# Optimization experiments

Hardware: AMD Instinct MI355X
Metric: run time of the kernel (lower is better)

Reference implementation:

```python
import jax, jax.numpy as jnp
import numpy as np

N = 50000      # nodes
E = 800000     # edges
INIT = 256     # input feature dim
HID = 64       # per-head hidden dim
EMB = 128      # output embed dim
H = 8          # heads
ALPHA = 0.2    # leaky-relu slope
EPS = 1e-16    # guard for isolated nodes


def setup_inputs() -> dict:
    key = jax.random.key(0)
    ks = jax.random.split(key, 6)
    x = jax.random.normal(ks[0], (N, INIT), dtype=jnp.float32)
    edge_index = jax.random.randint(ks[1], (2, E), 0, N, dtype=jnp.int32)
    # xavier-ish scaling keeps exp(-leakyrelu(.)) in a sane range
    W1 = jax.random.normal(ks[2], (H, INIT, HID), dtype=jnp.float32) / np.sqrt(INIT).astype(np.float32)
    a1 = jax.random.normal(ks[3], (H, 2 * HID), dtype=jnp.float32) / np.sqrt(2 * HID).astype(np.float32)
    Wo = jax.random.normal(ks[4], (H * HID, EMB), dtype=jnp.float32) / np.sqrt(H * HID).astype(np.float32)
    ao = jax.random.normal(ks[5], (2 * EMB,), dtype=jnp.float32) / np.sqrt(2 * EMB).astype(np.float32)
    return {"x": x, "edge_index": edge_index, "W1": W1, "a1": a1, "Wo": Wo, "ao": ao}


def _sp_att_head(x, W, a, src, dst):
    """One sparse GAT head (pyGAT SpGraphAttentionLayer math)."""
    h = x @ W                                              # [N, F']
    eh = jnp.concatenate([h[src], h[dst]], axis=1)          # [E, 2F']
    ee = jnp.exp(-jax.nn.leaky_relu(eh @ a, ALPHA))         # [E]
    denom = jax.ops.segment_sum(ee, src, num_segments=N) + EPS          # [N]
    num = jax.ops.segment_sum(ee[:, None] * h[dst], src, num_segments=N)  # [N, F']
    h_prime = num / denom[:, None]
    att = ee / denom[src]
    return h_prime, att


def reference(x, edge_index, W1, a1, Wo, ao, args=0):
    src, dst = edge_index[0], edge_index[1]
    # first (and only) multi-head layer, concat=True -> elu per head, concat on feature dim
    heads = [jax.nn.elu(_sp_att_head(x, W1[i], a1[i], src, dst)[0]) for i in range(H)]
    x1 = jnp.concatenate(heads, axis=1)                     # [N, H*HID]
    # output attention layer, concat=False; top-level applies elu
    h_prime, att_out = _sp_att_head(x1, Wo, ao, src, dst)
    return jax.nn.elu(h_prime), edge_index, att_out
```

## Files before the change

### kernel.cpp

```cpp
#include <hip/hip_runtime.h>
#include <hip/hip_bf16.h>
#include <cstddef>

#define NN    50000
#define NE    800000
#define FIN   256
#define HID   64
#define NH    8
#define F1    512
#define EMB   128
#define ALPHA 0.2f
#define EPSF  1e-16f
#define NBLK  ((NN + 255) / 256)

#if defined(__has_builtin)
# if __has_builtin(__builtin_amdgcn_cvt_scalef32_pk_f32_fp4) && __has_builtin(__builtin_amdgcn_cvt_scalef32_pk_fp4_f32)
#  define HAVE_FP4 1
# else
#  define HAVE_FP4 0
# endif
#else
# define HAVE_FP4 0
#endif

typedef __hip_bfloat16 bf16;
typedef __attribute__((ext_vector_type(8))) short short8;
typedef __attribute__((ext_vector_type(4))) float f32x4;
typedef __attribute__((ext_vector_type(2))) float f32x2;

#if HAVE_FP4
typedef uint2 pay_t;
#define PAYB1 (F1 / 2)
#define PAYB2 (EMB / 2)
#define SINV1 2.0f
#define SINV2 4.0f
#define PSC1  0.5f
#define PSC2  0.25f
#else
typedef uint4 pay_t;
#define PAYB1 F1
#define PAYB2 EMB
#define SINV1 1.0f
#define SINV2 1.0f
#define PSC1  1.0f
#define PSC2  1.0f
#endif

__device__ __forceinline__ float eluf(float x){ return x > 0.f ? x : __expf(x) - 1.f; }
__device__ __forceinline__ float lrelu_neg_exp(float s){
    float lr = s > 0.f ? s : ALPHA * s;
    return __expf(-lr);
}
__device__ __forceinline__ float b2f(unsigned u){ return __uint_as_float(u << 16); }

__device__ __forceinline__ void fma16pk(f32x2* acc, pay_t q, float e){
    f32x2 e2; e2[0] = e; e2[1] = e;
#if HAVE_FP4
    acc[0] += __builtin_amdgcn_cvt_scalef32_pk_f32_fp4(q.x, 1.0f, 0) * e2;
    acc[1] += __builtin_amdgcn_cvt_scalef32_pk_f32_fp4(q.x, 1.0f, 1) * e2;
    acc[2] += __builtin_amdgcn_cvt_scalef32_pk_f32_fp4(q.x, 1.0f, 2) * e2;
    acc[3] += __builtin_amdgcn_cvt_scalef32_pk_f32_fp4(q.x, 1.0f, 3) * e2;
    acc[4] += __builtin_amdgcn_cvt_scalef32_pk_f32_fp4(q.y, 1.0f, 0) * e2;
    acc[5] += __builtin_amdgcn_cvt_scalef32_pk_f32_fp4(q.y, 1.0f, 1) * e2;
    acc[6] += __builtin_amdgcn_cvt_scalef32_pk_f32_fp4(q.y, 1.0f, 2) * e2;
    acc[7] += __builtin_amdgcn_cvt_scalef32_pk_f32_fp4(q.y, 1.0f, 3) * e2;
#else
    acc[0] += __builtin_amdgcn_cvt_pk_f32_fp8(q.x, false) * e2;
    acc[1] += __builtin_amdgcn_cvt_pk_f32_fp8(q.x, true)  * e2;
    acc[2] += __builtin_amdgcn_cvt_pk_f32_fp8(q.y, false) * e2;
    acc[3] += __builtin_amdgcn_cvt_pk_f32_fp8(q.y, true)  * e2;
    acc[4] += __builtin_amdgcn_cvt_pk_f32_fp8(q.z, false) * e2;
    acc[5] += __builtin_amdgcn_cvt_pk_f32_fp8(q.z, true)  * e2;
    acc[6] += __builtin_amdgcn_cvt_pk_f32_fp8(q.w, false) * e2;
    acc[7] += __builtin_amdgcn_cvt_pk_f32_fp8(q.w, true)  * e2;
#endif
}

__device__ __forceinline__ unsigned bpack(float a, float b){
    unsigned ua = __float_as_uint(a), ub = __float_as_uint(b);
    ua = (ua + 0x7fffu + ((ua >> 16) & 1)) >> 16;
    ub = (ub + 0x7fffu + ((ub >> 16) & 1)) >> 16;
    return (ua & 0xffffu) | (ub << 16);
}

__global__ void k_tw1(const float* __restrict__ W1, bf16* __restrict__ Bt1){
    int i = blockIdx.x * 256 + threadIdx.x;
    if (i >= F1 * FIN) return;
    int n = i >> 8, k = i & 255;
    Bt1[i] = __float2bfloat16(W1[(size_t)(n >> 6) * FIN * HID + (size_t)k * HID + (n & 63)]);
}

__global__ void k_tw2(const float* __restrict__ Wo, bf16* __restrict__ WoT){
    int i = blockIdx.x * 256 + threadIdx.x;
    if (i >= EMB * F1) return;
    int n = i >> 9, k = i & 511;
    WoT[i] = __float2bfloat16(Wo[(size_t)k * EMB + n]);
}

__global__ void k_q4(const unsigned char* __restrict__ in, unsigned* __restrict__ out,
                     int n8, float sinv){
    int i = blockIdx.x * 256 + threadIdx.x;
    if (i >= n8) return;
    uint2 v = *(const uint2*)(in + (size_t)i * 8);
#if HAVE_FP4
    f32x2 a = __builtin_amdgcn_cvt_pk_f32_fp8(v.x, false);
    f32x2 b = __builtin_amdgcn_cvt_pk_f32_fp8(v.x, true);
    f32x2 c = __builtin_amdgcn_cvt_pk_f32_fp8(v.y, false);
    f32x2 d = __builtin_amdgcn_cvt_pk_f32_fp8(v.y, true);
    unsigned r = 0;
    r = __builtin_amdgcn_cvt_scalef32_pk_fp4_f32(r, a[0] * sinv, a[1] * sinv, 1.0f, 0);
    r = __builtin_amdgcn_cvt_scalef32_pk_fp4_f32(r, b[0] * sinv, b[1] * sinv, 1.0f, 1);
    r = __builtin_amdgcn_cvt_scalef32_pk_fp4_f32(r, c[0] * sinv, c[1] * sinv, 1.0f, 2);
    r = __builtin_amdgcn_cvt_scalef32_pk_fp4_f32(r, d[0] * sinv, d[1] * sinv, 1.0f, 3);
    out[i] = r;
#else
    (void)sinv;
    *(uint2*)((unsigned char*)out + (size_t)i * 8) = v;
#endif
}

__global__ void k_zero(int* p, int n){
    int i = blockIdx.x * 256 + threadIdx.x;
    if (i < n) p[i] = 0;
}

__global__ void k_count(const int* __restrict__ src, int* __restrict__ cnt){
    int e = blockIdx.x * 256 + threadIdx.x;
    if (e < NE) atomicAdd(&cnt[src[e]], 1);
}

__global__ __launch_bounds__(256) void k_bsum(const int* __restrict__ cnt, int* __restrict__ bsum){
    const int b = blockIdx.x, t = threadIdx.x, idx = b * 256 + t;
    int v = (idx < NN) ? cnt[idx] : 0;
#pragma unroll
    for (int o = 1; o < 64; o <<= 1) v += __shfl_xor(v, o);
    __shared__ int ws[4];
    if ((t & 63) == 0) ws[t >> 6] = v;
    __syncthreads();
    if (t == 0) bsum[b] = ws[0] + ws[1] + ws[2] + ws[3];
}

__global__ __launch_bounds__(256) void k_scanb(const int* __restrict__ bsum,
                                               int* __restrict__ boff,
                                               int* __restrict__ rp){
    const int t = threadIdx.x;
    __shared__ int s[256];
    const int v = (t < NBLK) ? bsum[t] : 0;
    s[t] = v;
    __syncthreads();
    for (int o = 1; o < 256; o <<= 1){
        int u = (t >= o) ? s[t - o] : 0;
        __syncthreads();
        s[t] += u;
        __syncthreads();
    }
    if (t < NBLK) boff[t] = s[t] - v;
    if (t == 255) rp[NN] = s[255];
}

__global__ __launch_bounds__(256) void k_rp(const int* __restrict__ cnt,
                                            const int* __restrict__ boff,
                                            int* __restrict__ rp){
    const int b = blockIdx.x, t = threadIdx.x, idx = b * 256 + t;
    const int v = (idx < NN) ? cnt[idx] : 0;
    __shared__ int s[256];
    s[t] = v;
    __syncthreads();
    for (int o = 1; o < 256; o <<= 1){
        int u = (t >= o) ? s[t - o] : 0;
        __syncthreads();
        s[t] += u;
        __syncthreads();
    }
    if (idx < NN) rp[idx] = boff[b] + s[t] - v;
}

__global__ void k_scatter_ee(const int* __restrict__ src, const int* __restrict__ dst,
                             const int* __restrict__ rp, int* __restrict__ cur,
                             const float* __restrict__ s11, const float* __restrict__ s12,
                             int* __restrict__ sdst, int* __restrict__ ssrc,
                             unsigned short* __restrict__ ee8b){
    int e = blockIdx.x * 256 + threadIdx.x;
    if (e >= NE) return;
    int s = src[e], d = dst[e];
    int p = atomicAdd(&cur[s], 1);
    int pos = rp[s] + p;
    sdst[pos] = d;
    ssrc[pos] = s;
    const float* ps = s11 + (size_t)s * NH;
    const float* pd = s12 + (size_t)d * NH;
    float w[8];
#pragma unroll
    for (int h = 0; h < 8; h++) w[h] = lrelu_neg_exp(ps[h] + pd[h]);
    uint4 o;
    o.x = bpack(w[0], w[1]); o.y = bpack(w[2], w[3]);
    o.z = bpack(w[4], w[5]); o.w = bpack(w[6], w[7]);
    *(uint4*)(ee8b + (size_t)pos * 8) = o;
}

__global__ void k_ee2(const int* __restrict__ ssrc, const int* __restrict__ sdst,
                      const float* __restrict__ s21, const float* __restrict__ s22,
                      float* __restrict__ ee2){
    int i = blockIdx.x * 256 + threadIdx.x;
    if (i >= NE) return;
    ee2[i] = lrelu_neg_exp(s21[ssrc[i]] + s22[sdst[i]]);
}

__global__ __launch_bounds__(256) void k_gemm1f(const float* __restrict__ A,
                                                const bf16* __restrict__ B,
                                                unsigned char* __restrict__ C){
    constexpr int K = FIN, N = F1;
    constexpr int LDT = 40;
    __shared__ __align__(16) bf16 As[128 * LDT];
    __shared__ __align__(16) bf16 Bs[128 * LDT];
    const int t = threadIdx.x;
    const int lane = t & 63, wid = t >> 6;
    const int m0 = blockIdx.x * 128, n0 = blockIdx.y * 128;
    const int r0 = t >> 2, u0 = t & 3;
    const int r1 = r0 + 64;
    const int rb = (wid & 1) * 64, cb = (wid >> 1) * 64;
    const int fr = lane & 15, fk = (lane >> 4) * 8;

    f32x4 acc[4][4];
#pragma unroll
    for (int i = 0; i < 4; i++)
#pragma unroll
        for (int j = 0; j < 4; j++) acc[i][j] = (f32x4)(0.f);

    for (int k0 = 0; k0 < K; k0 += 32){
        const int ga0 = m0 + r0, ga1 = m0 + r1;
        float4 a0a = make_float4(0,0,0,0), a0b = a0a, a1a = a0a, a1b = a0a;
        if (ga0 < NN){
            const float* p = A + (size_t)ga0 * K + k0 + u0 * 8;
            a0a = *(const float4*)p; a0b = *(const float4*)(p + 4);
        }
        if (ga1 < NN){
            const float* p = A + (size_t)ga1 * K + k0 + u0 * 8;
            a1a = *(const float4*)p; a1b = *(const float4*)(p + 4);
        }
        uint4 av0, av1;
        av0.x = bpack(a0a.x, a0a.y); av0.y = bpack(a0a.z, a0a.w);
        av0.z = bpack(a0b.x, a0b.y); av0.w = bpack(a0b.z, a0b.w);
        av1.x = bpack(a1a.x, a1a.y); av1.y = bpack(a1a.z, a1a.w);
        av1.z = bpack(a1b.x, a1b.y); av1.w = bpack(a1b.z, a1b.w);
        uint4 bv0 = *(const uint4*)(B + (size_t)(n0 + r0) * K + k0 + u0 * 8);
        uint4 bv1 = *(const uint4*)(B + (size_t)(n0 + r1) * K + k0 + u0 * 8);
        __syncthreads();
        *(uint4*)(As + r0 * LDT + u0 * 8) = av0;
        *(uint4*)(As + r1 * LDT + u0 * 8) = av1;
        *(uint4*)(Bs + r0 * LDT + u0 * 8) = bv0;
        *(uint4*)(Bs + r1 * LDT + u0 * 8) = bv1;
        __syncthreads();
        short8 af[4], bf_[4];
#pragma unroll
        for (int i = 0; i < 4; i++){
            af[i]  = *(const short8*)(As + (rb + i * 16 + fr) * LDT + fk);
            bf_[i] = *(const short8*)(Bs + (cb + i * 16 + fr) * LDT + fk);
        }
#pragma unroll
        for (int i = 0; i < 4; i++)
#pragma unroll
            for (int j = 0; j < 4; j++)
                acc[i][j] = __builtin_amdgcn_mfma_f32_16x16x32_bf16(af[i], bf_[j], acc[i][j], 0, 0, 0);
    }
    const int crow = m0 + rb + (lane >> 4) * 4;
    const int ccol = n0 + cb + (lane & 15);
#pragma unroll
    for (int i = 0; i < 4; i++)
#pragma unroll
        for (int j = 0; j < 4; j++)
#pragma unroll
            for (int v = 0; v < 4; v++){
                int row = crow + i * 16 + v;
                if (row < NN){
                    float val = acc[i][j][v];
                    unsigned r = __builtin_amdgcn_cvt_pk_fp8_f32(val, val, 0u, false);
                    C[(size_t)row * N + ccol + j * 16] = (unsigned char)(r & 0xffu);
                }
            }
}

__global__ __launch_bounds__(256) void k_gemm2n(const bf16* __restrict__ A,
                                                const bf16* __restrict__ B,
                                                unsigned char* __restrict__ C){
    constexpr int K = F1, N = EMB;
    constexpr int LDT = 40;
    __shared__ __align__(16) bf16 As[64 * LDT];
    __shared__ __align__(16) bf16 Bs[128 * LDT];
    const int t = threadIdx.x;
    const int lane = t & 63, wid = t >> 6;
    const int m0 = blockIdx.x * 64;
    const int r = t >> 2, u0 = t & 3;
    const int rb = (wid & 1) * 32, cb = (wid >> 1) * 64;
    const int fr = lane & 15, fk = (lane >> 4) * 8;

    f32x4 acc[2][4];
#pragma unroll
    for (int i = 0; i < 2; i++)
#pragma unroll
        for (int j = 0; j < 4; j++) acc[i][j] = (f32x4)(0.f);

    for (int k0 = 0; k0 < K; k0 += 32){
        const int ga = m0 + r;
        uint4 av = (ga < NN) ? *(const uint4*)(A + (size_t)ga * K + k0 + u0 * 8)
                             : make_uint4(0, 0, 0, 0);
        uint4 bv0 = *(const uint4*)(B + (size_t)r * K + k0 + u0 * 8);
        uint4 bv1 = *(const uint4*)(B + (size_t)(r + 64) * K + k0 + u0 * 8);
        __syncthreads();
        *(uint4*)(As + r * LDT + u0 * 8) = av;
        *(uint4*)(Bs + r * LDT + u0 * 8) = bv0;
        *(uint4*)(Bs + (r + 64) * LDT + u0 * 8) = bv1;
        __syncthreads();
        short8 af[2], bf_[4];
#pragma unroll
        for (int i = 0; i < 2; i++)
            af[i] = *(const short8*)(As + (rb + i * 16 + fr) * LDT + fk);
#pragma unroll
        for (int j = 0; j < 4; j++)
            bf_[j] = *(const short8*)(Bs + (cb + j * 16 + fr) * LDT + fk);
#pragma unroll
        for (int i = 0; i < 2; i++)
#pragma unroll
            for (int j = 0; j < 4; j++)
                acc[i][j] = __builtin_amdgcn_mfma_f32_16x16x32_bf16(af[i], bf_[j], acc[i][j], 0, 0, 0);
    }
    const int crow = m0 + rb + (lane >> 4) * 4;
    const int ccol = cb + (lane & 15);
#pragma unroll
    for (int i = 0; i < 2; i++)
#pragma unroll
        for (int j = 0; j < 4; j++)
#pragma unroll
            for (int v = 0; v < 4; v++){
                int row = crow + i * 16 + v;
                if (row < NN){
                    float val = acc[i][j][v];
                    unsigned r8 = __builtin_amdgcn_cvt_pk_fp8_f32(val, val, 0u, false);
                    C[(size_t)row * N + ccol + j * 16] = (unsigned char)(r8 & 0xffu);
                }
            }
}

__global__ void k_s1q(const unsigned char* __restrict__ h1q, const float* __restrict__ a1,
                      float* __restrict__ s11, float* __restrict__ s12,
                      unsigned char* __restrict__ pay){
    int idx = blockIdx.x * 256 + threadIdx.x;
    if (idx >= NN * NH) return;
    int n = idx >> 3, h = idx & 7;
    const uint4* hp = (const uint4*)(h1q + (size_t)n * F1 + h * HID);
    const float* a  = a1 + (size_t)h * 2 * HID;
    float d1 = 0.f, d2 = 0.f;
#if HAVE_FP4
    unsigned w8[8];
#endif
#pragma unroll
    for (int u = 0; u < 4; u++){
        uint4 q = hp[u];
        int j = u * 16;
        f32x2 p0 = __builtin_amdgcn_cvt_pk_f32_fp8(q.x, false);
        f32x2 p1 = __builtin_amdgcn_cvt_pk_f32_fp8(q.x, true);
        f32x2 p2 = __builtin_amdgcn_cvt_pk_f32_fp8(q.y, false);
        f32x2 p3 = __builtin_amdgcn_cvt_pk_f32_fp8(q.y, true);
        f32x2 p4 = __builtin_amdgcn_cvt_pk_f32_fp8(q.z, false);
        f32x2 p5 = __builtin_amdgcn_cvt_pk_f32_fp8(q.z, true);
        f32x2 p6 = __builtin_amdgcn_cvt_pk_f32_fp8(q.w, false);
        f32x2 p7 = __builtin_amdgcn_cvt_pk_f32_fp8(q.w, true);
        d1 += p0[0]*a[j+0] + p0[1]*a[j+1] + p1[0]*a[j+2] + p1[1]*a[j+3]
            + p2[0]*a[j+4] + p2[1]*a[j+5] + p3[0]*a[j+6] + p3[1]*a[j+7]
            + p4[0]*a[j+8] + p4[1]*a[j+9] + p5[0]*a[j+10]+ p5[1]*a[j+11]
            + p6[0]*a[j+12]+ p6[1]*a[j+13]+ p7[0]*a[j+14]+ p7[1]*a[j+15];
        d2 += p0[0]*a[HID+j+0] + p0[1]*a[HID+j+1] + p1[0]*a[HID+j+2] + p1[1]*a[HID+j+3]
            + p2[0]*a[HID+j+4] + p2[1]*a[HID+j+5] + p3[0]*a[HID+j+6] + p3[1]*a[HID+j+7]
            + p4[0]*a[HID+j+8] + p4[1]*a[HID+j+9] + p5[0]*a[HID+j+10]+ p5[1]*a[HID+j+11]
            + p6[0]*a[HID+j+12]+ p6[1]*a[HID+j+13]+ p7[0]*a[HID+j+14]+ p7[1]*a[HID+j+15];
#if HAVE_FP4
        unsigned r0 = 0, r1 = 0;
        r0 = __builtin_amdgcn_cvt_scalef32_pk_fp4_f32(r0, p0[0]*SINV1, p0[1]*SINV1, 1.0f, 0);
        r0 = __builtin_amdgcn_cvt_scalef32_pk_fp4_f32(r0, p1[0]*SINV1, p1[1]*SINV1, 1.0f, 1);
        r0 = __builtin_amdgcn_cvt_scalef32_pk_fp4_f32(r0, p2[0]*SINV1, p2[1]*SINV1, 1.0f, 2);
        r0 = __builtin_amdgcn_cvt_scalef32_pk_fp4_f32(r0, p3[0]*SINV1, p3[1]*SINV1, 1.0f, 3);
        r1 = __builtin_amdgcn_cvt_scalef32_pk_fp4_f32(r1, p4[0]*SINV1, p4[1]*SINV1, 1.0f, 0);
        r1 = __builtin_amdgcn_cvt_scalef32_pk_fp4_f32(r1, p5[0]*SINV1, p5[1]*SINV1, 1.0f, 1);
        r1 = __builtin_amdgcn_cvt_scalef32_pk_fp4_f32(r1, p6[0]*SINV1, p6[1]*SINV1, 1.0f, 2);
        r1 = __builtin_amdgcn_cvt_scalef32_pk_fp4_f32(r1, p7[0]*SINV1, p7[1]*SINV1, 1.0f, 3);
        w8[2 * u] = r0; w8[2 * u + 1] = r1;
#endif
    }
    s11[idx] = d1;
    s12[idx] = d2;
#if HAVE_FP4
    uint4* op = (uint4*)(pay + (size_t)n * PAYB1 + h * (HID / 2));
    uint4 o0, o1;
    o0.x = w8[0]; o0.y = w8[1]; o0.z = w8[2]; o0.w = w8[3];
    o1.x = w8[4]; o1.y = w8[5]; o1.z = w8[6]; o1.w = w8[7];
    op[0] = o0; op[1] = o1;
#else
    uint4* op = (uint4*)(pay + (size_t)n * PAYB1 + h * HID);
    op[0] = hp[0]; op[1] = hp[1]; op[2] = hp[2]; op[3] = hp[3];
#endif
}

__global__ __launch_bounds__(256) void k_agg1(const unsigned char* __restrict__ hq,
                                              const unsigned short* __restrict__ ee8b,
                                              const int* __restrict__ rp,
                                              const int* __restrict__ sdst,
                                              bf16* __restrict__ x1){
    const int t = threadIdx.x, lane = t & 63, w = t >> 6;
    const int n = blockIdx.x * 4 + w;
    const int l32 = lane & 31;
    const int half = lane >> 5;
    const int hf = l32 >> 2;
    const int eslot = lane >> 3;
    f32x2 acc[8];
#pragma unroll
    for (int i = 0; i < 8; i++){ acc[i][0] = 0.f; acc[i][1] = 0.f; }
    float dedp = 0.f;
    const int start = rp[n], end = rp[n + 1];
    const unsigned char* __restrict__ hl = hq + (size_t)l32 * (PAYB1 / 32);
    for (int c0 = start; c0 < end; c0 += 64){
        const int m = min(64, end - c0);
        int dreg = (lane < m) ? sdst[c0 + lane] : 0;
        for (int g = 0; g * 8 < m; g++){
            unsigned short eu = ee8b[(size_t)(c0 + g * 8) * 8 + lane];
            dedp += (g * 8 + eslot < m) ? b2f(eu) : 0.f;
        }
        for (int j = 0; j < m; j += 16){
            int dj[8]; unsigned short eu[8]; pay_t q[8];
#pragma unroll
            for (int p = 0; p < 8; p++){
                const int e2 = j + 2 * p + half;
                dj[p] = __shfl(dreg, e2);
                eu[p] = ee8b[(size_t)(c0 + e2) * 8 + hf];
                q[p]  = *(const pay_t*)(hl + (size_t)dj[p] * PAYB1);
            }
#pragma unroll
            for (int p = 0; p < 8; p++){
                const int e2 = j + 2 * p + half;
                const float e = (e2 < m) ? b2f(eu[p]) : 0.f;
                fma16pk(acc, q[p], e);
            }
        }
    }
    dedp += __shfl_xor(dedp, 8);
    dedp += __shfl_xor(dedp, 16);
    dedp += __shfl_xor(dedp, 32);
#pragma unroll
    for (int i = 0; i < 8; i++){
        acc[i][0] += __shfl_xor(acc[i][0], 32);
        acc[i][1] += __shfl_xor(acc[i][1], 32);
    }
    float ded = __shfl(dedp, hf);
    const float inv = PSC1 / (ded + EPSF);
    if (half == 0){
        float o[16];
#pragma unroll
        for (int i = 0; i < 8; i++){
            o[2 * i]     = eluf(acc[i][0] * inv);
            o[2 * i + 1] = eluf(acc[i][1] * inv);
        }
        uint4 ov0, ov1;
        ov0.x = bpack(o[0], o[1]);   ov0.y = bpack(o[2], o[3]);
        ov0.z = bpack(o[4], o[5]);   ov0.w = bpack(o[6], o[7]);
        ov1.x = bpack(o[8], o[9]);   ov1.y = bpack(o[10], o[11]);
        ov1.z = bpack(o[12], o[13]); ov1.w = bpack(o[14], o[15]);
        bf16* xp = x1 + (size_t)n * F1 + l32 * 16;
        *(uint4*)xp = ov0;
        *(uint4*)(xp + 8) = ov1;
    }
}

__global__ void k_s2(const unsigned char* __restrict__ h2q, const float* __restrict__ ao,
                     float* __restrict__ s21, float* __restrict__ s22){
    int n = blockIdx.x * 256 + threadIdx.x;
    if (n >= NN) return;
    const uint4* hp = (const uint4*)(h2q + (size_t)n * EMB);
    float d1 = 0.f, d2 = 0.f;
#pragma unroll
    for (int u = 0; u < 8; u++){
        uint4 q = hp[u];
        int j = u * 16;
#define S2(w, o) { f32x2 p0 = __builtin_amdgcn_cvt_pk_f32_fp8((w), false); \
                   f32x2 p1 = __builtin_amdgcn_cvt_pk_f32_fp8((w), true); \
                   d1 += p0[0]*ao[(o)] + p0[1]*ao[(o)+1] + p1[0]*ao[(o)+2] + p1[1]*ao[(o)+3]; \
                   d2 += p0[0]*ao[EMB+(o)] + p0[1]*ao[EMB+(o)+1] + p1[0]*ao[EMB+(o)+2] + p1[1]*ao[EMB+(o)+3]; }
        S2(q.x, j) S2(q.y, j + 4) S2(q.z, j + 8) S2(q.w, j + 12)
#undef S2
    }
    s21[n] = d1;
    s22[n] = d2;
}

__global__ __launch_bounds__(256) void k_agg2(const unsigned char* __restrict__ hq,
                                              const float* __restrict__ ee2,
                                              const int* __restrict__ rp,
                                              const int* __restrict__ sdst,
                                              float* __restrict__ den2,
                                              float* __restrict__ out0){
    const int t = threadIdx.x, lane = t & 63, w = t >> 6;
    const int n = blockIdx.x * 4 + w;
    const int slot = lane >> 3;
    const int fpos = lane & 7;
    f32x2 acc[8];
#pragma unroll
    for (int i = 0; i < 8; i++){ acc[i][0] = 0.f; acc[i][1] = 0.f; }
    float dedp = 0.f;
    const int start = rp[n], end = rp[n + 1];
    const unsigned char* __restrict__ hl = hq + (size_t)fpos * (PAYB2 / 8);
    for (int c0 = start; c0 < end; c0 += 64){
        const int m = min(64, end - c0);
        int dreg = (lane < m) ? sdst[c0 + lane] : 0;
        float ev = (lane < m) ? ee2[c0 + lane] : 0.f;
        dedp += ev;
        for (int j = 0; j < m; j += 8){
            const int ei = j + slot;
            const float e = __shfl(ev, ei);
            const int   d = __shfl(dreg, ei);
            pay_t q = *(const pay_t*)(hl + (size_t)d * PAYB2);
            fma16pk(acc, q, e);
        }
    }
#pragma unroll
    for (int o = 1; o <= 32; o <<= 1) dedp += __shfl_xor(dedp, o);
#pragma unroll
    for (int o = 8; o <= 32; o <<= 1)
#pragma unroll
        for (int i = 0; i < 8; i++){
            acc[i][0] += __shfl_xor(acc[i][0], o);
            acc[i][1] += __shfl_xor(acc[i][1], o);
        }
    const float den = dedp + EPSF;
    if (slot == 0){
        const float inv = PSC2 / den;
        float* op = out0 + (size_t)n * EMB + fpos * 16;
#pragma unroll
        for (int u = 0; u < 4; u++){
            float4 ov;
            ov.x = eluf(acc[2 * u][0] * inv);
            ov.y = eluf(acc[2 * u][1] * inv);
            ov.z = eluf(acc[2 * u + 1][0] * inv);
            ov.w = eluf(acc[2 * u + 1][1] * inv);
            *(float4*)(op + u * 4) = ov;
        }
        if (lane == 0) den2[n] = den;
    }
}

__global__ void k_att_edge4(const int* __restrict__ ei,
                            const float* __restrict__ s21, const float* __restrict__ s22,
                            const float* __restrict__ den2,
                            float* __restrict__ outE, float* __restrict__ outA){
    int i = blockIdx.x * 256 + threadIdx.x;
    if (i >= NE / 4) return;
    int4 s4 = ((const int4*)ei)[i];
    int4 d4 = ((const int4*)(ei + NE))[i];
    float4 fs = make_float4((float)s4.x, (float)s4.y, (float)s4.z, (float)s4.w);
    float4 fd = make_float4((float)d4.x, (float)d4.y, (float)d4.z, (float)d4.w);
    ((float4*)outE)[i] = fs;
    ((float4*)(outE + NE))[i] = fd;
    float4 av;
    av.x = lrelu_neg_exp(s21[s4.x] + s22[d4.x]) / den2[s4.x];
    av.y = lrelu_neg_exp(s21[s4.y] + s22[d4.y]) / den2[s4.y];
    av.z = lrelu_neg_exp(s21[s4.z] + s22[d4.z]) / den2[s4.z];
    av.w = lrelu_neg_exp(s21[s4.w] + s22[d4.w]) / den2[s4.w];
    ((float4*)outA)[i] = av;
}

extern "C" void kernel_launch(void* const* d_in, const int* in_sizes, int n_in,
                              void* d_out, int out_size, void* d_ws, size_t ws_size,
                              hipStream_t stream){
    const float* x  = (const float*)d_in[0];
    const int*   ei = (const int*)d_in[1];
    const float* W1 = (const float*)d_in[2];
    const float* a1 = (const float*)d_in[3];
    const float* Wo = (const float*)d_in[4];
    const float* ao = (const float*)d_in[5];
    float* out = (float*)d_out;
    const int* src = ei;
    const int* dst = ei + NE;

    char* w = (char*)d_ws;
    auto alloc = [&](size_t bytes) -> char* {
        char* p = w;
        w += (bytes + 255) & ~(size_t)255;
        return p;
    };
    unsigned char* h1pay = (unsigned char*)alloc((size_t)NN * F1);
    bf16*  x1   = (bf16*) alloc((size_t)NN * F1 * 2);
    unsigned char* h1q = (unsigned char*)alloc((size_t)NN * F1);
    unsigned char* h2q = (unsigned char*)alloc((size_t)NN * EMB);
    unsigned short* ee8b = (unsigned short*)alloc(((size_t)NE + 64) * 8 * 2);
    float* ee2  = (float*)alloc((size_t)NE * 4);
    bf16*  Bt1  = (bf16*) alloc((size_t)F1 * FIN * 2);
    bf16*  WoT  = (bf16*) alloc((size_t)EMB * F1 * 2);
    float* s11  = (float*)alloc((size_t)NN * NH * 4);
    float* s12  = (float*)alloc((size_t)NN * NH * 4);
    float* s21  = (float*)alloc((size_t)NN * 4);
    float* s22  = (float*)alloc((size_t)NN * 4);
    float* den2 = (float*)alloc((size_t)NN * 4);
    int*   cnt2 = (int*)  alloc((size_t)2 * NN * 4);
    int*   rp   = (int*)  alloc((size_t)(NN + 1) * 4);
    int*   sdst = (int*)  alloc((size_t)NE * 4);
    int*   ssrc = (int*)  alloc((size_t)NE * 4);
    int*   bsum = (int*)  alloc((size_t)NBLK * 4);
    int*   boff = (int*)  alloc((size_t)NBLK * 4);
    int*   cnt = cnt2;
    int*   cur = cnt2 + NN;
    unsigned char* h2pay = (unsigned char*)x1;

    k_tw1<<<(F1 * FIN + 255) / 256, 256, 0, stream>>>(W1, Bt1);
    k_tw2<<<(EMB * F1 + 255) / 256, 256, 0, stream>>>(Wo, WoT);

    k_zero <<<(2 * NN + 255) / 256, 256, 0, stream>>>(cnt2, 2 * NN);
    k_count<<<(NE + 255) / 256,     256, 0, stream>>>(src, cnt);
    k_bsum <<<NBLK,                 256, 0, stream>>>(cnt, bsum);
    k_scanb<<<1,                    256, 0, stream>>>(bsum, boff, rp);
    k_rp   <<<NBLK,                 256, 0, stream>>>(cnt, boff, rp);

    k_gemm1f<<<dim3((NN + 127) / 128, F1 / 128), 256, 0, stream>>>(x, Bt1, h1q);
    k_s1q <<<(NN * NH + 255) / 256, 256, 0, stream>>>(h1q, a1, s11, s12, h1pay);
    k_scatter_ee<<<(NE + 255) / 256, 256, 0, stream>>>(src, dst, rp, cur, s11, s12,
                                                       sdst, ssrc, ee8b);
    k_agg1<<<NN / 4, 256, 0, stream>>>(h1pay, ee8b, rp, sdst, x1);

    k_gemm2n<<<(NN + 63) / 64, 256, 0, stream>>>(x1, WoT, h2q);
    k_q4  <<<(NN * EMB / 8 + 255) / 256, 256, 0, stream>>>(h2q, (unsigned*)h2pay, NN * EMB / 8, SINV2);
    k_s2  <<<(NN + 255) / 256, 256, 0, stream>>>(h2q, ao, s21, s22);
    k_ee2 <<<(NE + 255) / 256, 256, 0, stream>>>(ssrc, sdst, s21, s22, ee2);
    k_agg2<<<NN / 4, 256, 0, stream>>>(h2pay, ee2, rp, sdst, den2, out);

    k_att_edge4<<<(NE / 4 + 255) / 256, 256, 0, stream>>>(ei, s21, s22, den2,
                                                          out + (size_t)NN * EMB,
                                                          out + (size_t)NN * EMB + 2 * NE);
}
```

Measured before the change: 319.7 us.

## Pack per-edge CSR data into interleaved 32-byte records

Replaces the separate sorted dst, src, bf16 attention and layer-2 score arrays with one 32-byte record per sorted edge holding dst, src, the layer-2 score and eight packed layer-1 weights. The scatter, ee2 and both aggregation kernels read and write these records, so each edge's data comes from one or two adjacent 16-byte loads instead of several arrays. Layer-1 denominators are now summed per head across the whole wave and then selected, rather than reduced with a strided layout. In exchange the per-edge footprint grows to 32 bytes, with padding, so total traffic may rise. The per-head bf16 reads in k_agg1 now stride 32 bytes instead of 16.

```diff
diff --git a/kernel.cpp b/kernel.cpp
--- a/kernel.cpp
+++ b/kernel.cpp
@@ -45,6 +45,8 @@
 #define PSC1  1.0f
 #define PSC2  1.0f
 #endif
+
+#define RECB 32
 
 __device__ __forceinline__ float eluf(float x){ return x > 0.f ? x : __expf(x) - 1.f; }
 __device__ __forceinline__ float lrelu_neg_exp(float s){
@@ -178,32 +180,35 @@
 __global__ void k_scatter_ee(const int* __restrict__ src, const int* __restrict__ dst,
                              const int* __restrict__ rp, int* __restrict__ cur,
                              const float* __restrict__ s11, const float* __restrict__ s12,
-                             int* __restrict__ sdst, int* __restrict__ ssrc,
-                             unsigned short* __restrict__ ee8b){
+                             unsigned char* __restrict__ rec){
     int e = blockIdx.x * 256 + threadIdx.x;
     if (e >= NE) return;
     int s = src[e], d = dst[e];
-    int p = atomicAdd(&cur[s], 1);
-    int pos = rp[s] + p;
-    sdst[pos] = d;
-    ssrc[pos] = s;
     const float* ps = s11 + (size_t)s * NH;
     const float* pd = s12 + (size_t)d * NH;
     float w[8];
 #pragma unroll
     for (int h = 0; h < 8; h++) w[h] = lrelu_neg_exp(ps[h] + pd[h]);
-    uint4 o;
-    o.x = bpack(w[0], w[1]); o.y = bpack(w[2], w[3]);
-    o.z = bpack(w[4], w[5]); o.w = bpack(w[6], w[7]);
-    *(uint4*)(ee8b + (size_t)pos * 8) = o;
-}
-
-__global__ void k_ee2(const int* __restrict__ ssrc, const int* __restrict__ sdst,
-                      const float* __restrict__ s21, const float* __restrict__ s22,
-                      float* __restrict__ ee2){
+    uint4 rB;
+    rB.x = bpack(w[0], w[1]); rB.y = bpack(w[2], w[3]);
+    rB.z = bpack(w[4], w[5]); rB.w = bpack(w[6], w[7]);
+    uint4 rA;
+    rA.x = (unsigned)d; rA.y = (unsigned)s; rA.z = 0u; rA.w = 0u;
+    int p = atomicAdd(&cur[s], 1);
+    size_t pos = (size_t)rp[s] + p;
+    uint4* rq = (uint4*)(rec + pos * RECB);
+    rq[0] = rA;
+    rq[1] = rB;
+}
+
+__global__ void k_ee2(unsigned char* __restrict__ rec,
+                      const float* __restrict__ s21, const float* __restrict__ s22){
     int i = blockIdx.x * 256 + threadIdx.x;
     if (i >= NE) return;
-    ee2[i] = lrelu_neg_exp(s21[ssrc[i]] + s22[sdst[i]]);
+    const uint4 rA = *(const uint4*)(rec + (size_t)i * RECB);
+    int d = (int)rA.x, s = (int)rA.y;
+    float v = lrelu_neg_exp(s21[s] + s22[d]);
+    *(float*)(rec + (size_t)i * RECB + 8) = v;
 }
 
 __global__ __launch_bounds__(256) void k_gemm1f(const float* __restrict__ A,
@@ -401,36 +406,42 @@
 }
 
 __global__ __launch_bounds__(256) void k_agg1(const unsigned char* __restrict__ hq,
-                                              const unsigned short* __restrict__ ee8b,
+                                              const unsigned char* __restrict__ rec,
                                               const int* __restrict__ rp,
-                                              const int* __restrict__ sdst,
                                               bf16* __restrict__ x1){
     const int t = threadIdx.x, lane = t & 63, w = t >> 6;
     const int n = blockIdx.x * 4 + w;
     const int l32 = lane & 31;
     const int half = lane >> 5;
     const int hf = l32 >> 2;
-    const int eslot = lane >> 3;
     f32x2 acc[8];
 #pragma unroll
     for (int i = 0; i < 8; i++){ acc[i][0] = 0.f; acc[i][1] = 0.f; }
-    float dedp = 0.f;
+    float ded8[8];
+#pragma unroll
+    for (int h = 0; h < 8; h++) ded8[h] = 0.f;
     const int start = rp[n], end = rp[n + 1];
     const unsigned char* __restrict__ hl = hq + (size_t)l32 * (PAYB1 / 32);
     for (int c0 = start; c0 < end; c0 += 64){
         const int m = min(64, end - c0);
-        int dreg = (lane < m) ? sdst[c0 + lane] : 0;
-        for (int g = 0; g * 8 < m; g++){
-            unsigned short eu = ee8b[(size_t)(c0 + g * 8) * 8 + lane];
-            dedp += (g * 8 + eslot < m) ? b2f(eu) : 0.f;
-        }
+        uint4 rA = make_uint4(0, 0, 0, 0), rB = make_uint4(0, 0, 0, 0);
+        if (lane < m){
+            const uint4* rq = (const uint4*)(rec + (size_t)(c0 + lane) * RECB);
+            rA = rq[0];
+            rB = rq[1];
+        }
+        const int dreg = (int)rA.x;
+        ded8[0] += b2f(rB.x & 0xffffu); ded8[1] += b2f(rB.x >> 16);
+        ded8[2] += b2f(rB.y & 0xffffu); ded8[3] += b2f(rB.y >> 16);
+        ded8[4] += b2f(rB.z & 0xffffu); ded8[5] += b2f(rB.z >> 16);
+        ded8[6] += b2f(rB.w & 0xffffu); ded8[7] += b2f(rB.w >> 16);
         for (int j = 0; j < m; j += 16){
             int dj[8]; unsigned short eu[8]; pay_t q[8];
 #pragma unroll
             for (int p = 0; p < 8; p++){
                 const int e2 = j + 2 * p + half;
                 dj[p] = __shfl(dreg, e2);
-                eu[p] = ee8b[(size_t)(c0 + e2) * 8 + hf];
+                eu[p] = *(const unsigned short*)(rec + (size_t)(c0 + e2) * RECB + 16 + hf * 2);
                 q[p]  = *(const pay_t*)(hl + (size_t)dj[p] * PAYB1);
             }
 #pragma unroll
@@ -441,15 +452,19 @@
             }
         }
     }
-    dedp += __shfl_xor(dedp, 8);
-    dedp += __shfl_xor(dedp, 16);
-    dedp += __shfl_xor(dedp, 32);
+#pragma unroll
+    for (int h = 0; h < 8; h++){
+#pragma unroll
+        for (int o = 1; o <= 32; o <<= 1) ded8[h] += __shfl_xor(ded8[h], o);
+    }
 #pragma unroll
     for (int i = 0; i < 8; i++){
         acc[i][0] += __shfl_xor(acc[i][0], 32);
         acc[i][1] += __shfl_xor(acc[i][1], 32);
     }
-    float ded = __shfl(dedp, hf);
+    float ded = ded8[0];
+#pragma unroll
+    for (int h = 1; h < 8; h++) ded = (hf == h) ? ded8[h] : ded;
     const float inv = PSC1 / (ded + EPSF);
     if (half == 0){
         float o[16];
@@ -491,9 +506,8 @@
 }
 
 __global__ __launch_bounds__(256) void k_agg2(const unsigned char* __restrict__ hq,
-                                              const float* __restrict__ ee2,
+                                              const unsigned char* __restrict__ rec,
                                               const int* __restrict__ rp,
-                                              const int* __restrict__ sdst,
                                               float* __restrict__ den2,
                                               float* __restrict__ out0){
     const int t = threadIdx.x, lane = t & 63, w = t >> 6;
@@ -508,8 +522,10 @@
     const unsigned char* __restrict__ hl = hq + (size_t)fpos * (PAYB2 / 8);
     for (int c0 = start; c0 < end; c0 += 64){
         const int m = min(64, end - c0);
-        int dreg = (lane < m) ? sdst[c0 + lane] : 0;
-        float ev = (lane < m) ? ee2[c0 + lane] : 0.f;
+        uint4 rA = make_uint4(0, 0, 0, 0);
+        if (lane < m) rA = *(const uint4*)(rec + (size_t)(c0 + lane) * RECB);
+        const int dreg = (int)rA.x;
+        const float ev = __uint_as_float(rA.z);
         dedp += ev;
         for (int j = 0; j < m; j += 8){
             const int ei = j + slot;
@@ -584,12 +600,11 @@
         w += (bytes + 255) & ~(size_t)255;
         return p;
     };
-    unsigned char* h1pay = (unsigned char*)alloc((size_t)NN * F1);
+    unsigned char* h1pay = (unsigned char*)alloc((size_t)NN * PAYB1);
     bf16*  x1   = (bf16*) alloc((size_t)NN * F1 * 2);
     unsigned char* h1q = (unsigned char*)alloc((size_t)NN * F1);
     unsigned char* h2q = (unsigned char*)alloc((size_t)NN * EMB);
-    unsigned short* ee8b = (unsigned short*)alloc(((size_t)NE + 64) * 8 * 2);
-    float* ee2  = (float*)alloc((size_t)NE * 4);
+    unsigned char* rec = (unsigned char*)alloc(((size_t)NE + 64) * RECB);
     bf16*  Bt1  = (bf16*) alloc((size_t)F1 * FIN * 2);
     bf16*  WoT  = (bf16*) alloc((size_t)EMB * F1 * 2);
     float* s11  = (float*)alloc((size_t)NN * NH * 4);
@@ -599,8 +614,6 @@
     float* den2 = (float*)alloc((size_t)NN * 4);
     int*   cnt2 = (int*)  alloc((size_t)2 * NN * 4);
     int*   rp   = (int*)  alloc((size_t)(NN + 1) * 4);
-    int*   sdst = (int*)  alloc((size_t)NE * 4);
-    int*   ssrc = (int*)  alloc((size_t)NE * 4);
     int*   bsum = (int*)  alloc((size_t)NBLK * 4);
     int*   boff = (int*)  alloc((size_t)NBLK * 4);
     int*   cnt = cnt2;
@@ -618,15 +631,14 @@
 
     k_gemm1f<<<dim3((NN + 127) / 128, F1 / 128), 256, 0, stream>>>(x, Bt1, h1q);
     k_s1q <<<(NN * NH + 255) / 256, 256, 0, stream>>>(h1q, a1, s11, s12, h1pay);
-    k_scatter_ee<<<(NE + 255) / 256, 256, 0, stream>>>(src, dst, rp, cur, s11, s12,
-                                                       sdst, ssrc, ee8b);
-    k_agg1<<<NN / 4, 256, 0, stream>>>(h1pay, ee8b, rp, sdst, x1);
+    k_scatter_ee<<<(NE + 255) / 256, 256, 0, stream>>>(src, dst, rp, cur, s11, s12, rec);
+    k_agg1<<<NN / 4, 256, 0, stream>>>(h1pay, rec, rp, x1);
 
     k_gemm2n<<<(NN + 63) / 64, 256, 0, stream>>>(x1, WoT, h2q);
     k_q4  <<<(NN * EMB / 8 + 255) / 256, 256, 0, stream>>>(h2q, (unsigned*)h2pay, NN * EMB / 8, SINV2);
     k_s2  <<<(NN + 255) / 256, 256, 0, stream>>>(h2q, ao, s21, s22);
-    k_ee2 <<<(NE + 255) / 256, 256, 0, stream>>>(ssrc, sdst, s21, s22, ee2);
-    k_agg2<<<NN / 4, 256, 0, stream>>>(h2pay, ee2, rp, sdst, den2, out);
+    k_ee2 <<<(NE + 255) / 256, 256, 0, stream>>>(rec, s21, s22);
+    k_agg2<<<NN / 4, 256, 0, stream>>>(h2pay, rec, rp, den2, out);
 
     k_att_edge4<<<(NE / 4 + 255) / 256, 256, 0, stream>>>(ei, s21, s22, den2,
                                                           out + (size_t)NN * EMB,
```

Result: no change. 320.2 us (+0.2%).
